# Kernel tuning notes

Hardware: AMD Instinct MI355X
Metric: run time of the kernel (lower is better)

## Reference

```python
import jax, jax.numpy as jnp
import numpy as np

N_NODES = 40000
N_EDGES = 640000
N_GRAPHS = 64
D_IN = 128
D_H = 128
N_LAYERS = 3
EPS = 1e-5


def _layer_norm(x, g, b):
    mu = jnp.mean(x, axis=-1, keepdims=True)
    var = jnp.var(x, axis=-1, keepdims=True)
    return (x - mu) * jax.lax.rsqrt(var + EPS) * g + b


def _sage_conv(x, src, dst, Wl, bl, Wr):
    # mean aggregation of neighbor messages: i <- mean_{j: (j->i)} x_j
    msg = x[src]                                              # [E, d]
    agg = jax.ops.segment_sum(msg, dst, num_segments=N_NODES)  # [N, d]
    deg = jax.ops.segment_sum(jnp.ones((src.shape[0],), x.dtype), dst,
                              num_segments=N_NODES)
    agg = agg / jnp.clip(deg, 1.0)[:, None]
    # out = lin_l(agg) + lin_r(x)
    return agg @ Wl.T + bl + x @ Wr.T


def setup_inputs() -> dict:
    key = jax.random.key(0)
    ks = jax.random.split(key, 12)
    s = 0.05
    x = jax.random.normal(ks[0], (N_NODES, D_IN), jnp.float32)
    edge_index = jax.random.randint(ks[1], (2, N_EDGES), 0, N_NODES, jnp.int64)
    batch = jnp.sort(jax.random.randint(ks[2], (N_NODES,), 0, N_GRAPHS, jnp.int64))
    fc_w = jax.random.normal(ks[3], (D_H, D_IN), jnp.float32) * s
    fc_b = jax.random.normal(ks[4], (D_H,), jnp.float32) * s
    Wl = jax.random.normal(ks[5], (N_LAYERS, D_H, D_H), jnp.float32) * s
    bl = jax.random.normal(ks[6], (N_LAYERS, D_H), jnp.float32) * s
    Wr = jax.random.normal(ks[7], (N_LAYERS, D_H, D_H), jnp.float32) * s
    ln_g = jnp.ones((N_LAYERS - 1, D_H), jnp.float32)
    ln_b = jnp.zeros((N_LAYERS - 1, D_H), jnp.float32)
    return {"x": x, "edge_index": edge_index, "batch": batch,
            "fc_w": fc_w, "fc_b": fc_b, "Wl": Wl, "bl": bl, "Wr": Wr,
            "ln_g": ln_g, "ln_b": ln_b}


def reference(x, edge_index, batch, fc_w, fc_b, Wl, bl, Wr, ln_g, ln_b):
    src, dst = edge_index[0], edge_index[1]
    # input projection + ReLU
    h = jax.nn.relu(x @ fc_w.T + fc_b)
    # GraphSAGE stack: norm + ReLU between layers, none after the last
    for i in range(N_LAYERS):
        h = _sage_conv(h, src, dst, Wl[i], bl[i], Wr[i])
        if i < N_LAYERS - 1:
            h = jax.nn.relu(_layer_norm(h, ln_g[i], ln_b[i]))
    node_embed = h                                            # [N, D_H]
    graph_embed = jax.ops.segment_sum(node_embed, batch,
                                      num_segments=N_GRAPHS)  # [G, D_H]
    return node_embed, graph_embed
```

## Files before the change

kernel.cpp:

```cpp
#include <hip/hip_runtime.h>
#include <hip/hip_bf16.h>


#define N_NODES 40000
#define N_EDGES 640000
#define N_GRAPHS 64
#define D 128
#define NODE_ELEMS 5120000
#define N_TILES 1250
#define ELL_W 64

typedef __hip_bfloat16 bf16;
typedef __attribute__((ext_vector_type(8))) short bf16x8;
typedef __attribute__((ext_vector_type(4))) float f32x4;

__device__ __forceinline__ float b2f(bf16 v) { return __bfloat162float(v); }
__device__ __forceinline__ bf16 f2b(float v) { return __float2bfloat16(v); }
__device__ __forceinline__ unsigned packbf(float a, float b) {
    union { bf16 h[2]; unsigned u; } c;
    c.h[0] = f2b(a); c.h[1] = f2b(b);
    return c.u;
}
__device__ __forceinline__ unsigned char f2e4m3(float v) {
    unsigned u = __float_as_uint(v * 0x1p-120f);
    unsigned r = (u + 0x0007ffffu + ((u >> 20) & 1u)) >> 20;
    return (unsigned char)min(r, 0x7eu);
}
__device__ __forceinline__ int is_bf16(const unsigned* lng) {
    return (lng[0] == 0x3f803f80u) ? 1 : 0;
}
__device__ __forceinline__ int edge_is_i64(const void* edge) {
    const unsigned* ew = (const unsigned*)edge;
    return (ew[1] == 0u && ew[3] == 0u && ew[5] == 0u) ? 1 : 0;
}

union U8 { uint4 u; bf16x8 s; };

template <int ISB>
__device__ __forceinline__ bf16x8 load8t(const void* base, long idx) {
    if (ISB) {
        U8 t;
        t.u = *(const uint4*)((const bf16*)base + idx);
        return t.s;
    }
    const float* f = (const float*)base + idx;
    float4 f0 = *(const float4*)f;
    float4 f1 = *(const float4*)(f + 4);
    union { bf16 h[8]; bf16x8 s; } t;
    t.h[0] = f2b(f0.x); t.h[1] = f2b(f0.y); t.h[2] = f2b(f0.z); t.h[3] = f2b(f0.w);
    t.h[4] = f2b(f1.x); t.h[5] = f2b(f1.y); t.h[6] = f2b(f1.z); t.h[7] = f2b(f1.w);
    return t.s;
}

template <int ISB>
__device__ __forceinline__ void proj_body(
    const void* __restrict__ X, const void* __restrict__ fcw,
    const void* __restrict__ fcb, bf16* __restrict__ outb,
    unsigned char* __restrict__ out8, int id, int t,
    bf16 (*sb)[128], unsigned char (*s8)[128]) {
    const int lane = t & 63;
    const int wave = t >> 6;
    const int n = lane & 15, q = lane >> 4;
    const int rowgrp = wave >> 1;
    const int cb = (wave & 1) * 64;
    const f32x4 zero = {0.f, 0.f, 0.f, 0.f};

    bf16x8 wf[4][4];
#pragma unroll
    for (int ct = 0; ct < 4; ct++)
#pragma unroll
        for (int ks = 0; ks < 4; ks++)
            wf[ct][ks] = load8t<ISB>(fcw, (long)(cb + ct * 16 + n) * 128 + ks * 32 + q * 8);
    float bz[4];
#pragma unroll
    for (int ct = 0; ct < 4; ct++)
        bz[ct] = ISB ? b2f(((const bf16*)fcb)[cb + ct * 16 + n])
                     : ((const float*)fcb)[cb + ct * 16 + n];

    for (int tile = id; tile < N_TILES; tile += 512) {
        const long rbase = (long)tile * 32 + rowgrp * 16 + n;
        f32x4 acc[4] = {zero, zero, zero, zero};
        bf16x8 af[4];
#pragma unroll
        for (int ks = 0; ks < 4; ks++)
            af[ks] = load8t<ISB>(X, rbase * 128 + ks * 32 + q * 8);
#pragma unroll
        for (int ct = 0; ct < 4; ct++)
#pragma unroll
            for (int ks = 0; ks < 4; ks++)
                acc[ct] = __builtin_amdgcn_mfma_f32_16x16x32_bf16(
                    af[ks], wf[ct][ks], acc[ct], 0, 0, 0);
#pragma unroll
        for (int ct = 0; ct < 4; ct++) {
            const int col = cb + ct * 16 + n;
#pragma unroll
            for (int r = 0; r < 4; r++) {
                const int rl = rowgrp * 16 + q * 4 + r;
                float v = fmaxf(acc[ct][r] + bz[ct], 0.f);
                sb[rl][col] = f2b(v);
                s8[rl][col] = f2e4m3(v);
            }
        }
        __syncthreads();
        {
            uint4* ob = (uint4*)((char*)outb + (size_t)tile * 8192);
            ob[t] = ((const uint4*)sb)[t];
            ob[t + 256] = ((const uint4*)sb)[t + 256];
            ((uint4*)(out8 + (size_t)tile * 4096))[t] = ((const uint4*)s8)[t];
        }
        __syncthreads();
    }
}

#define CW2_TOTAL 99200
__global__ __launch_bounds__(256, 4) void k_main(
    const void* __restrict__ X, const void* __restrict__ fcw,
    const void* __restrict__ fcb, bf16* __restrict__ outb,
    unsigned char* __restrict__ out8,
    const void* __restrict__ edge, const void* __restrict__ batch,
    const void* Wl, const void* bl, const void* Wr,
    const void* lng, const void* lnb,
    int* __restrict__ cursor, unsigned short* __restrict__ ell,
    int* __restrict__ batch32, bf16* __restrict__ cw,
    float* __restrict__ gsum) {
    __shared__ bf16 sb[32][128];
    __shared__ unsigned char s8[32][128];
    const int bid = blockIdx.x, t = threadIdx.x;
    int role, id;
    if (bid < 1000) { role = (bid & 1) ? 0 : 1; id = bid >> 1; }
    else if (bid < 1012) { role = 0; id = 500 + (bid - 1000); }
    else if (bid < 1169) { role = 2; id = bid - 1012; }
    else { role = 3; id = bid - 1169; }

    if (role == 1) {
        const int i64 = edge_is_i64(edge);
        int s[5], d[5];
#pragma unroll
        for (int i = 0; i < 5; i++) {
            int e = id * 1280 + i * 256 + t;
            if (i64) {
                s[i] = (int)((const long long*)edge)[e];
                d[i] = (int)((const long long*)edge)[N_EDGES + e];
            } else {
                s[i] = ((const int*)edge)[e];
                d[i] = ((const int*)edge)[N_EDGES + e];
            }
        }
        int p[5];
#pragma unroll
        for (int i = 0; i < 5; i++) p[i] = atomicAdd(&cursor[d[i]], 1);
#pragma unroll
        for (int i = 0; i < 5; i++)
            if (p[i] < ELL_W) ell[d[i] * ELL_W + p[i]] = (unsigned short)s[i];
        return;
    }
    if (role == 2) {
        int j = id * 256 + t;
        if (j < N_NODES)
            batch32[j] = edge_is_i64(edge) ? (int)((const long long*)batch)[j]
                                           : ((const int*)batch)[j];
        return;
    }
    if (role == 3) {
        int i = id * 256 + t;
        if (i >= CW2_TOTAL) return;
        int isb = is_bf16((const unsigned*)lng);
        const void* s; int o;
        if (i < 49152)       { s = Wl;  o = i; }
        else if (i < 49536)  { s = bl;  o = i - 49152; }
        else if (i < 98688)  { s = Wr;  o = i - 49536; }
        else if (i < 98944)  { s = lng; o = i - 98688; }
        else                 { s = lnb; o = i - 98944; }
        cw[i] = isb ? ((const bf16*)s)[o] : f2b(((const float*)s)[o]);
        return;
    }

    {
        int i = id * 256 + t;
        if (i < N_GRAPHS * D) gsum[i] = 0.f;
    }
    if (is_bf16((const unsigned*)lng))
        proj_body<1>(X, fcw, fcb, outb, out8, id, t, sb, s8);
    else
        proj_body<0>(X, fcw, fcb, outb, out8, id, t, sb, s8);
}

__global__ __launch_bounds__(256, 6) void k_agg8(
    const unsigned char* __restrict__ h8, const int* __restrict__ cursor,
    const unsigned short* __restrict__ ell, bf16* __restrict__ agg) {
    const int qw = threadIdx.x >> 4;
    const int l16 = threadIdx.x & 15;
    const int nodeA = blockIdx.x * 32 + qw * 2;
    const int nodeB = nodeA + 1;
    const int degA = min(cursor[nodeA], ELL_W);
    const int degB = min(cursor[nodeB], ELL_W);
    const int dmax = max(degA, degB);
    const uint4* rA = (const uint4*)(ell + (size_t)nodeA * ELL_W);
    const uint4* rB = (const uint4*)(ell + (size_t)nodeB * ELL_W);
    const uint2* hp = (const uint2*)h8;
    float aA[8] = {0.f, 0.f, 0.f, 0.f, 0.f, 0.f, 0.f, 0.f};
    float aB[8] = {0.f, 0.f, 0.f, 0.f, 0.f, 0.f, 0.f, 0.f};
    for (int e = 0; e < dmax; e += 8) {
        const uint4 ia = rA[e >> 3];
        const uint4 ib = rB[e >> 3];
        uint2 gA[8], gB[8];
        gA[0] = hp[(size_t)(ia.x & 0xffffu) * 16 + l16];
        gA[1] = hp[(size_t)(ia.x >> 16) * 16 + l16];
        gA[2] = hp[(size_t)(ia.y & 0xffffu) * 16 + l16];
        gA[3] = hp[(size_t)(ia.y >> 16) * 16 + l16];
        gA[4] = hp[(size_t)(ia.z & 0xffffu) * 16 + l16];
        gA[5] = hp[(size_t)(ia.z >> 16) * 16 + l16];
        gA[6] = hp[(size_t)(ia.w & 0xffffu) * 16 + l16];
        gA[7] = hp[(size_t)(ia.w >> 16) * 16 + l16];
        gB[0] = hp[(size_t)(ib.x & 0xffffu) * 16 + l16];
        gB[1] = hp[(size_t)(ib.x >> 16) * 16 + l16];
        gB[2] = hp[(size_t)(ib.y & 0xffffu) * 16 + l16];
        gB[3] = hp[(size_t)(ib.y >> 16) * 16 + l16];
        gB[4] = hp[(size_t)(ib.z & 0xffffu) * 16 + l16];
        gB[5] = hp[(size_t)(ib.z >> 16) * 16 + l16];
        gB[6] = hp[(size_t)(ib.w & 0xffffu) * 16 + l16];
        gB[7] = hp[(size_t)(ib.w >> 16) * 16 + l16];
#pragma unroll
        for (int i = 0; i < 8; i++) {
            const float mA = (e + i < degA) ? 0x1p120f : 0.f;
            aA[0] = fmaf(mA, __uint_as_float((gA[i].x << 20) & 0x07f00000u), aA[0]);
            aA[1] = fmaf(mA, __uint_as_float((gA[i].x << 12) & 0x07f00000u), aA[1]);
            aA[2] = fmaf(mA, __uint_as_float((gA[i].x << 4)  & 0x07f00000u), aA[2]);
            aA[3] = fmaf(mA, __uint_as_float((gA[i].x >> 4)  & 0x07f00000u), aA[3]);
            aA[4] = fmaf(mA, __uint_as_float((gA[i].y << 20) & 0x07f00000u), aA[4]);
            aA[5] = fmaf(mA, __uint_as_float((gA[i].y << 12) & 0x07f00000u), aA[5]);
            aA[6] = fmaf(mA, __uint_as_float((gA[i].y << 4)  & 0x07f00000u), aA[6]);
            aA[7] = fmaf(mA, __uint_as_float((gA[i].y >> 4)  & 0x07f00000u), aA[7]);
        }
#pragma unroll
        for (int i = 0; i < 8; i++) {
            const float mB = (e + i < degB) ? 0x1p120f : 0.f;
            aB[0] = fmaf(mB, __uint_as_float((gB[i].x << 20) & 0x07f00000u), aB[0]);
            aB[1] = fmaf(mB, __uint_as_float((gB[i].x << 12) & 0x07f00000u), aB[1]);
            aB[2] = fmaf(mB, __uint_as_float((gB[i].x << 4)  & 0x07f00000u), aB[2]);
            aB[3] = fmaf(mB, __uint_as_float((gB[i].x >> 4)  & 0x07f00000u), aB[3]);
            aB[4] = fmaf(mB, __uint_as_float((gB[i].y << 20) & 0x07f00000u), aB[4]);
            aB[5] = fmaf(mB, __uint_as_float((gB[i].y << 12) & 0x07f00000u), aB[5]);
            aB[6] = fmaf(mB, __uint_as_float((gB[i].y << 4)  & 0x07f00000u), aB[6]);
            aB[7] = fmaf(mB, __uint_as_float((gB[i].y >> 4)  & 0x07f00000u), aB[7]);
        }
    }
    const float invA = 1.f / (float)max(degA, 1);
    const float invB = 1.f / (float)max(degB, 1);
    uint4 oA, oB;
    oA.x = packbf(aA[0] * invA, aA[1] * invA);
    oA.y = packbf(aA[2] * invA, aA[3] * invA);
    oA.z = packbf(aA[4] * invA, aA[5] * invA);
    oA.w = packbf(aA[6] * invA, aA[7] * invA);
    oB.x = packbf(aB[0] * invB, aB[1] * invB);
    oB.y = packbf(aB[2] * invB, aB[3] * invB);
    oB.z = packbf(aB[4] * invB, aB[5] * invB);
    oB.w = packbf(aB[6] * invB, aB[7] * invB);
    ((uint4*)agg)[(size_t)nodeA * 16 + l16] = oA;
    ((uint4*)agg)[(size_t)nodeB * 16 + l16] = oB;
}

template <int MODE>
__global__ __launch_bounds__(256, 2) void k_gemm(
    const bf16* __restrict__ A, const bf16* __restrict__ W1,
    const bf16* __restrict__ B, const bf16* __restrict__ W2,
    const bf16* __restrict__ bias, bf16* __restrict__ outb,
    unsigned char* __restrict__ out8, void* __restrict__ outx,
    const bf16* __restrict__ lgam, const bf16* __restrict__ lbet,
    const unsigned* __restrict__ lngraw) {
    __shared__ float sred[2][2][16][2];
    __shared__ bf16 sb[32][128];
    __shared__ unsigned char s8[32][128];
    __shared__ float sf[32][128];
    const int tid = threadIdx.x;
    const int lane = tid & 63;
    const int wave = tid >> 6;
    const int n = lane & 15, q = lane >> 4;
    const int rowgrp = wave >> 1;
    const int cbi = wave & 1;
    const int cb = cbi * 64;
    const int isb = is_bf16(lngraw);

    bf16x8 wf[2][4][4];
#pragma unroll
    for (int p = 0; p < 2; p++) {
        const bf16* Wp = p ? W2 : W1;
#pragma unroll
        for (int ct = 0; ct < 4; ct++)
#pragma unroll
            for (int ks = 0; ks < 4; ks++) {
                U8 t;
                t.u = *(const uint4*)&Wp[(cb + ct * 16 + n) * 128 + ks * 32 + q * 8];
                wf[p][ct][ks] = t.s;
            }
    }
    float bz[4], gf[4], bf_[4];
#pragma unroll
    for (int ct = 0; ct < 4; ct++) {
        bz[ct] = b2f(bias[cb + ct * 16 + n]);
        if (MODE == 1) {
            gf[ct] = b2f(lgam[cb + ct * 16 + n]);
            bf_[ct] = b2f(lbet[cb + ct * 16 + n]);
        }
    }

    const f32x4 zero = {0.f, 0.f, 0.f, 0.f};

    for (int tile = blockIdx.x; tile < N_TILES; tile += gridDim.x) {
        const long rbase = (long)tile * 32 + rowgrp * 16 + n;
        f32x4 acc[4] = {zero, zero, zero, zero};
#pragma unroll
        for (int p = 0; p < 2; p++) {
            const bf16* Ap = p ? B : A;
            bf16x8 af[4];
#pragma unroll
            for (int ks = 0; ks < 4; ks++) {
                U8 t;
                t.u = *(const uint4*)&Ap[rbase * 128 + ks * 32 + q * 8];
                af[ks] = t.s;
            }
#pragma unroll
            for (int ct = 0; ct < 4; ct++)
#pragma unroll
                for (int ks = 0; ks < 4; ks++)
                    acc[ct] = __builtin_amdgcn_mfma_f32_16x16x32_bf16(
                        af[ks], wf[p][ct][ks], acc[ct], 0, 0, 0);
        }

        float vs[4][4];
#pragma unroll
        for (int ct = 0; ct < 4; ct++)
#pragma unroll
            for (int r = 0; r < 4; r++) vs[ct][r] = acc[ct][r] + bz[ct];

        if (MODE == 1) {
            float s[4], ss[4];
#pragma unroll
            for (int r = 0; r < 4; r++) {
                s[r] = 0.f; ss[r] = 0.f;
#pragma unroll
                for (int ct = 0; ct < 4; ct++) {
                    s[r] += vs[ct][r];
                    ss[r] += vs[ct][r] * vs[ct][r];
                }
            }
#pragma unroll
            for (int m = 1; m <= 8; m <<= 1)
#pragma unroll
                for (int r = 0; r < 4; r++) {
                    s[r] += __shfl_xor(s[r], m, 64);
                    ss[r] += __shfl_xor(ss[r], m, 64);
                }
            if (n == 0) {
#pragma unroll
                for (int r = 0; r < 4; r++) {
                    sred[rowgrp][cbi][q * 4 + r][0] = s[r];
                    sred[rowgrp][cbi][q * 4 + r][1] = ss[r];
                }
            }
            __syncthreads();
#pragma unroll
            for (int r = 0; r < 4; r++) {
                float S = s[r] + sred[rowgrp][1 - cbi][q * 4 + r][0];
                float SS = ss[r] + sred[rowgrp][1 - cbi][q * 4 + r][1];
                float mu = S * (1.f / 128.f);
                float var = SS * (1.f / 128.f) - mu * mu;
                float rstd = rsqrtf(var + 1e-5f);
#pragma unroll
                for (int ct = 0; ct < 4; ct++)
                    vs[ct][r] = fmaxf((vs[ct][r] - mu) * rstd * gf[ct] + bf_[ct], 0.f);
            }
        }

#pragma unroll
        for (int ct = 0; ct < 4; ct++) {
            const int col = cb + ct * 16 + n;
#pragma unroll
            for (int r = 0; r < 4; r++) {
                const int rl = rowgrp * 16 + q * 4 + r;
                float v = vs[ct][r];
                if (MODE == 1) {
                    sb[rl][col] = f2b(v);
                    s8[rl][col] = f2e4m3(v);
                } else {
                    if (isb) sb[rl][col] = f2b(v);
                    else sf[rl][col] = v;
                }
            }
        }
        __syncthreads();
        if (MODE == 1) {
            uint4* ob = (uint4*)((char*)outb + (size_t)tile * 8192);
            ob[tid] = ((const uint4*)sb)[tid];
            ob[tid + 256] = ((const uint4*)sb)[tid + 256];
            ((uint4*)(out8 + (size_t)tile * 4096))[tid] = ((const uint4*)s8)[tid];
        } else {
            if (isb) {
                uint4* ob = (uint4*)((char*)outx + (size_t)tile * 8192);
                ob[tid] = ((const uint4*)sb)[tid];
                ob[tid + 256] = ((const uint4*)sb)[tid + 256];
            } else {
                uint4* of = (uint4*)((char*)outx + (size_t)tile * 16384);
#pragma unroll
                for (int k = 0; k < 4; k++)
                    of[tid + 256 * k] = ((const uint4*)sf)[tid + 256 * k];
            }
        }
        __syncthreads();
    }
}

__device__ __forceinline__ int lbound(const int* a, int n, int key) {
    int lo = 0, hi = n;
    while (lo < hi) {
        int mid = (lo + hi) >> 1;
        if (a[mid] < key) lo = mid + 1; else hi = mid;
    }
    return lo;
}

__global__ void k_graph(const void* __restrict__ node, const int* __restrict__ batch,
                        float* __restrict__ gsum, const unsigned* __restrict__ lngraw) {
    const int g = blockIdx.x >> 4, part = blockIdx.x & 15;
    const int c = threadIdx.x;
    const int isb = is_bf16(lngraw);
    const int lo = lbound(batch, N_NODES, g);
    const int hi = lbound(batch, N_NODES, g + 1);
    const int len = hi - lo;
    const int b0 = lo + (len * part) / 16;
    const int b1 = lo + (len * (part + 1)) / 16;
    float s0 = 0.f, s1 = 0.f;
    int n = b0;
    if (isb) {
        const bf16* nb = (const bf16*)node;
        for (; n + 2 <= b1; n += 2) {
            s0 += b2f(nb[(size_t)(n + 0) * 128 + c]);
            s1 += b2f(nb[(size_t)(n + 1) * 128 + c]);
        }
        for (; n < b1; n++) s0 += b2f(nb[(size_t)n * 128 + c]);
    } else {
        const float* nf = (const float*)node;
        for (; n + 2 <= b1; n += 2) {
            s0 += nf[(size_t)(n + 0) * 128 + c];
            s1 += nf[(size_t)(n + 1) * 128 + c];
        }
        for (; n < b1; n++) s0 += nf[(size_t)n * 128 + c];
    }
    atomicAdd(&gsum[g * 128 + c], s0 + s1);
}

__global__ void k_gout(const float* __restrict__ gsum, void* __restrict__ out,
                       const unsigned* __restrict__ lngraw) {
    int i = blockIdx.x * 256 + threadIdx.x;
    if (i >= N_GRAPHS * D) return;
    if (is_bf16(lngraw)) ((bf16*)out)[NODE_ELEMS + i] = f2b(gsum[i]);
    else ((float*)out)[NODE_ELEMS + i] = gsum[i];
}

extern "C" void kernel_launch(void* const* d_in, const int* in_sizes, int n_in,
                              void* d_out, int out_size, void* d_ws, size_t ws_size,
                              hipStream_t stream) {
    const void* x = d_in[0];
    const void* edge = d_in[1];
    const void* batch = d_in[2];
    const void* fc_w = d_in[3];
    const void* fc_b = d_in[4];
    const void* Wl = d_in[5];
    const void* bl = d_in[6];
    const void* Wr = d_in[7];
    const void* ln_g = d_in[8];
    const void* ln_b = d_in[9];
    const unsigned* lngraw = (const unsigned*)ln_g;

    size_t off = 0;
    char* base = (char*)d_ws;
    auto carve = [&](size_t bytes) -> char* {
        char* p = base + off;
        off = (off + bytes + 255) & ~(size_t)255;
        return p;
    };
    bf16* cw = (bf16*)carve((size_t)CW2_TOTAL * 2);
    bf16* hA = (bf16*)carve((size_t)NODE_ELEMS * 2);
    bf16* hB = (bf16*)carve((size_t)NODE_ELEMS * 2);
    bf16* agg = (bf16*)carve((size_t)NODE_ELEMS * 2);
    unsigned char* h8A = (unsigned char*)carve((size_t)NODE_ELEMS);
    unsigned char* h8B = (unsigned char*)carve((size_t)NODE_ELEMS);
    int* batch32 = (int*)carve((size_t)N_NODES * 4);
    unsigned short* ell = (unsigned short*)carve((size_t)N_NODES * ELL_W * 2);
    int* cursor = (int*)carve((size_t)N_NODES * 4);
    float* gsum = (float*)carve((size_t)N_GRAPHS * D * 4);

    const bf16* cw_Wl = cw;
    const bf16* cw_bl = cw + 49152;
    const bf16* cw_Wr = cw + 49536;
    const bf16* cw_lng = cw + 98688;
    const bf16* cw_lnb = cw + 98944;

    hipMemsetAsync(cursor, 0, (size_t)N_NODES * 4, stream);
    k_main<<<1557, 256, 0, stream>>>(x, fc_w, fc_b, hA, h8A, edge, batch,
                                     Wl, bl, Wr, ln_g, ln_b,
                                     cursor, ell, batch32, cw, gsum);

    bf16* hcur = hA;
    bf16* hnext = hB;
    unsigned char* h8cur = h8A;
    unsigned char* h8next = h8B;
    for (int l = 0; l < 3; l++) {
        const bf16* W1 = cw_Wl + (size_t)l * 16384;
        const bf16* W2 = cw_Wr + (size_t)l * 16384;
        const bf16* bb = cw_bl + (size_t)l * 128;
        k_agg8<<<1250, 256, 0, stream>>>(h8cur, cursor, ell, agg);
        if (l < 2) {
            k_gemm<1><<<512, 256, 0, stream>>>(agg, W1, hcur, W2, bb, hnext,
                                               h8next, nullptr,
                                               cw_lng + (size_t)l * 128,
                                               cw_lnb + (size_t)l * 128, lngraw);
            bf16* t = hcur; hcur = hnext; hnext = t;
            unsigned char* t8 = h8cur; h8cur = h8next; h8next = t8;
        } else {
            k_gemm<2><<<512, 256, 0, stream>>>(agg, W1, hcur, W2, bb, nullptr,
                                               nullptr, d_out, nullptr, nullptr,
                                               lngraw);
        }
    }

    k_graph<<<1024, 128, 0, stream>>>(d_out, batch32, gsum, lngraw);
    k_gout<<<32, 256, 0, stream>>>(gsum, d_out, lngraw);
}
```

Measured before the change: 241.4 us.

## Store hidden states and aggregates in 8-bit float, dropping bf16 copies

Removes the bf16 copies of the node features and of the aggregated messages. Every intermediate (projection output, layer outputs, neighbor means) is now kept only in a custom 8-bit e4m3-like format and decoded to bf16 in registers before the MFMA GEMMs. This roughly halves the bytes written and read per layer in the GEMM and aggregation kernels. The cost is reduced precision for the self term and the aggregate, plus some decode ALU work in the GEMM load path.

```diff
diff --git a/kernel.cpp b/kernel.cpp
--- a/kernel.cpp
+++ b/kernel.cpp
@@ -16,11 +16,6 @@
 
 __device__ __forceinline__ float b2f(bf16 v) { return __bfloat162float(v); }
 __device__ __forceinline__ bf16 f2b(float v) { return __float2bfloat16(v); }
-__device__ __forceinline__ unsigned packbf(float a, float b) {
-    union { bf16 h[2]; unsigned u; } c;
-    c.h[0] = f2b(a); c.h[1] = f2b(b);
-    return c.u;
-}
 __device__ __forceinline__ unsigned char f2e4m3(float v) {
     unsigned u = __float_as_uint(v * 0x1p-120f);
     unsigned r = (u + 0x0007ffffu + ((u >> 20) & 1u)) >> 20;
@@ -35,6 +30,21 @@
 }
 
 union U8 { uint4 u; bf16x8 s; };
+
+__device__ __forceinline__ bf16x8 dec8(uint2 w) {
+    union { unsigned short us[8]; bf16x8 s; } o;
+#pragma unroll
+    for (int i = 0; i < 4; i++) {
+        unsigned b = (w.x >> (8 * i)) & 0xffu;
+        o.us[i] = b ? (unsigned short)((b + 960u) << 4) : (unsigned short)0;
+    }
+#pragma unroll
+    for (int i = 0; i < 4; i++) {
+        unsigned b = (w.y >> (8 * i)) & 0xffu;
+        o.us[4 + i] = b ? (unsigned short)((b + 960u) << 4) : (unsigned short)0;
+    }
+    return o.s;
+}
 
 template <int ISB>
 __device__ __forceinline__ bf16x8 load8t(const void* base, long idx) {
@@ -55,9 +65,8 @@
 template <int ISB>
 __device__ __forceinline__ void proj_body(
     const void* __restrict__ X, const void* __restrict__ fcw,
-    const void* __restrict__ fcb, bf16* __restrict__ outb,
-    unsigned char* __restrict__ out8, int id, int t,
-    bf16 (*sb)[128], unsigned char (*s8)[128]) {
+    const void* __restrict__ fcb, unsigned char* __restrict__ out8,
+    int id, int t, unsigned char (*s8)[128]) {
     const int lane = t & 63;
     const int wave = t >> 6;
     const int n = lane & 15, q = lane >> 4;
@@ -96,18 +105,11 @@
 #pragma unroll
             for (int r = 0; r < 4; r++) {
                 const int rl = rowgrp * 16 + q * 4 + r;
-                float v = fmaxf(acc[ct][r] + bz[ct], 0.f);
-                sb[rl][col] = f2b(v);
-                s8[rl][col] = f2e4m3(v);
+                s8[rl][col] = f2e4m3(fmaxf(acc[ct][r] + bz[ct], 0.f));
             }
         }
         __syncthreads();
-        {
-            uint4* ob = (uint4*)((char*)outb + (size_t)tile * 8192);
-            ob[t] = ((const uint4*)sb)[t];
-            ob[t + 256] = ((const uint4*)sb)[t + 256];
-            ((uint4*)(out8 + (size_t)tile * 4096))[t] = ((const uint4*)s8)[t];
-        }
+        ((uint4*)(out8 + (size_t)tile * 4096))[t] = ((const uint4*)s8)[t];
         __syncthreads();
     }
 }
@@ -115,15 +117,13 @@
 #define CW2_TOTAL 99200
 __global__ __launch_bounds__(256, 4) void k_main(
     const void* __restrict__ X, const void* __restrict__ fcw,
-    const void* __restrict__ fcb, bf16* __restrict__ outb,
-    unsigned char* __restrict__ out8,
+    const void* __restrict__ fcb, unsigned char* __restrict__ out8,
     const void* __restrict__ edge, const void* __restrict__ batch,
     const void* Wl, const void* bl, const void* Wr,
     const void* lng, const void* lnb,
     int* __restrict__ cursor, unsigned short* __restrict__ ell,
     int* __restrict__ batch32, bf16* __restrict__ cw,
     float* __restrict__ gsum) {
-    __shared__ bf16 sb[32][128];
     __shared__ unsigned char s8[32][128];
     const int bid = blockIdx.x, t = threadIdx.x;
     int role, id;
@@ -180,14 +180,14 @@
         if (i < N_GRAPHS * D) gsum[i] = 0.f;
     }
     if (is_bf16((const unsigned*)lng))
-        proj_body<1>(X, fcw, fcb, outb, out8, id, t, sb, s8);
+        proj_body<1>(X, fcw, fcb, out8, id, t, s8);
     else
-        proj_body<0>(X, fcw, fcb, outb, out8, id, t, sb, s8);
+        proj_body<0>(X, fcw, fcb, out8, id, t, s8);
 }
 
 __global__ __launch_bounds__(256, 6) void k_agg8(
     const unsigned char* __restrict__ h8, const int* __restrict__ cursor,
-    const unsigned short* __restrict__ ell, bf16* __restrict__ agg) {
+    const unsigned short* __restrict__ ell, unsigned char* __restrict__ agg8) {
     const int qw = threadIdx.x >> 4;
     const int l16 = threadIdx.x & 15;
     const int nodeA = blockIdx.x * 32 + qw * 2;
@@ -247,30 +247,29 @@
     }
     const float invA = 1.f / (float)max(degA, 1);
     const float invB = 1.f / (float)max(degB, 1);
-    uint4 oA, oB;
-    oA.x = packbf(aA[0] * invA, aA[1] * invA);
-    oA.y = packbf(aA[2] * invA, aA[3] * invA);
-    oA.z = packbf(aA[4] * invA, aA[5] * invA);
-    oA.w = packbf(aA[6] * invA, aA[7] * invA);
-    oB.x = packbf(aB[0] * invB, aB[1] * invB);
-    oB.y = packbf(aB[2] * invB, aB[3] * invB);
-    oB.z = packbf(aB[4] * invB, aB[5] * invB);
-    oB.w = packbf(aB[6] * invB, aB[7] * invB);
-    ((uint4*)agg)[(size_t)nodeA * 16 + l16] = oA;
-    ((uint4*)agg)[(size_t)nodeB * 16 + l16] = oB;
+    uint2 oA, oB;
+    oA.x = (unsigned)f2e4m3(aA[0] * invA) | ((unsigned)f2e4m3(aA[1] * invA) << 8) |
+           ((unsigned)f2e4m3(aA[2] * invA) << 16) | ((unsigned)f2e4m3(aA[3] * invA) << 24);
+    oA.y = (unsigned)f2e4m3(aA[4] * invA) | ((unsigned)f2e4m3(aA[5] * invA) << 8) |
+           ((unsigned)f2e4m3(aA[6] * invA) << 16) | ((unsigned)f2e4m3(aA[7] * invA) << 24);
+    oB.x = (unsigned)f2e4m3(aB[0] * invB) | ((unsigned)f2e4m3(aB[1] * invB) << 8) |
+           ((unsigned)f2e4m3(aB[2] * invB) << 16) | ((unsigned)f2e4m3(aB[3] * invB) << 24);
+    oB.y = (unsigned)f2e4m3(aB[4] * invB) | ((unsigned)f2e4m3(aB[5] * invB) << 8) |
+           ((unsigned)f2e4m3(aB[6] * invB) << 16) | ((unsigned)f2e4m3(aB[7] * invB) << 24);
+    ((uint2*)agg8)[(size_t)nodeA * 16 + l16] = oA;
+    ((uint2*)agg8)[(size_t)nodeB * 16 + l16] = oB;
 }
 
 template <int MODE>
 __global__ __launch_bounds__(256, 2) void k_gemm(
-    const bf16* __restrict__ A, const bf16* __restrict__ W1,
-    const bf16* __restrict__ B, const bf16* __restrict__ W2,
-    const bf16* __restrict__ bias, bf16* __restrict__ outb,
-    unsigned char* __restrict__ out8, void* __restrict__ outx,
-    const bf16* __restrict__ lgam, const bf16* __restrict__ lbet,
-    const unsigned* __restrict__ lngraw) {
+    const unsigned char* __restrict__ A8, const bf16* __restrict__ W1,
+    const unsigned char* __restrict__ B8, const bf16* __restrict__ W2,
+    const bf16* __restrict__ bias, unsigned char* __restrict__ out8,
+    void* __restrict__ outx, const bf16* __restrict__ lgam,
+    const bf16* __restrict__ lbet, const unsigned* __restrict__ lngraw) {
     __shared__ float sred[2][2][16][2];
+    __shared__ unsigned char s8[32][128];
     __shared__ bf16 sb[32][128];
-    __shared__ unsigned char s8[32][128];
     __shared__ float sf[32][128];
     const int tid = threadIdx.x;
     const int lane = tid & 63;
@@ -311,14 +310,11 @@
         f32x4 acc[4] = {zero, zero, zero, zero};
 #pragma unroll
         for (int p = 0; p < 2; p++) {
-            const bf16* Ap = p ? B : A;
+            const unsigned char* Ap = p ? B8 : A8;
             bf16x8 af[4];
 #pragma unroll
-            for (int ks = 0; ks < 4; ks++) {
-                U8 t;
-                t.u = *(const uint4*)&Ap[rbase * 128 + ks * 32 + q * 8];
-                af[ks] = t.s;
-            }
+            for (int ks = 0; ks < 4; ks++)
+                af[ks] = dec8(*(const uint2*)&Ap[rbase * 128 + ks * 32 + q * 8]);
 #pragma unroll
             for (int ct = 0; ct < 4; ct++)
 #pragma unroll
@@ -380,7 +376,6 @@
                 const int rl = rowgrp * 16 + q * 4 + r;
                 float v = vs[ct][r];
                 if (MODE == 1) {
-                    sb[rl][col] = f2b(v);
                     s8[rl][col] = f2e4m3(v);
                 } else {
                     if (isb) sb[rl][col] = f2b(v);
@@ -390,9 +385,6 @@
         }
         __syncthreads();
         if (MODE == 1) {
-            uint4* ob = (uint4*)((char*)outb + (size_t)tile * 8192);
-            ob[tid] = ((const uint4*)sb)[tid];
-            ob[tid + 256] = ((const uint4*)sb)[tid + 256];
             ((uint4*)(out8 + (size_t)tile * 4096))[tid] = ((const uint4*)s8)[tid];
         } else {
             if (isb) {
@@ -480,9 +472,7 @@
         return p;
     };
     bf16* cw = (bf16*)carve((size_t)CW2_TOTAL * 2);
-    bf16* hA = (bf16*)carve((size_t)NODE_ELEMS * 2);
-    bf16* hB = (bf16*)carve((size_t)NODE_ELEMS * 2);
-    bf16* agg = (bf16*)carve((size_t)NODE_ELEMS * 2);
+    unsigned char* agg8 = (unsigned char*)carve((size_t)NODE_ELEMS);
     unsigned char* h8A = (unsigned char*)carve((size_t)NODE_ELEMS);
     unsigned char* h8B = (unsigned char*)carve((size_t)NODE_ELEMS);
     int* batch32 = (int*)carve((size_t)N_NODES * 4);
@@ -497,30 +487,26 @@
     const bf16* cw_lnb = cw + 98944;
 
     hipMemsetAsync(cursor, 0, (size_t)N_NODES * 4, stream);
-    k_main<<<1557, 256, 0, stream>>>(x, fc_w, fc_b, hA, h8A, edge, batch,
+    k_main<<<1557, 256, 0, stream>>>(x, fc_w, fc_b, h8A, edge, batch,
                                      Wl, bl, Wr, ln_g, ln_b,
                                      cursor, ell, batch32, cw, gsum);
 
-    bf16* hcur = hA;
-    bf16* hnext = hB;
     unsigned char* h8cur = h8A;
     unsigned char* h8next = h8B;
     for (int l = 0; l < 3; l++) {
         const bf16* W1 = cw_Wl + (size_t)l * 16384;
         const bf16* W2 = cw_Wr + (size_t)l * 16384;
         const bf16* bb = cw_bl + (size_t)l * 128;
-        k_agg8<<<1250, 256, 0, stream>>>(h8cur, cursor, ell, agg);
+        k_agg8<<<1250, 256, 0, stream>>>(h8cur, cursor, ell, agg8);
         if (l < 2) {
-            k_gemm<1><<<512, 256, 0, stream>>>(agg, W1, hcur, W2, bb, hnext,
-                                               h8next, nullptr,
+            k_gemm<1><<<512, 256, 0, stream>>>(agg8, W1, h8cur, W2, bb, h8next,
+                                               nullptr,
                                                cw_lng + (size_t)l * 128,
                                                cw_lnb + (size_t)l * 128, lngraw);
-            bf16* t = hcur; hcur = hnext; hnext = t;
             unsigned char* t8 = h8cur; h8cur = h8next; h8next = t8;
         } else {
-            k_gemm<2><<<512, 256, 0, stream>>>(agg, W1, hcur, W2, bb, nullptr,
-                                               nullptr, d_out, nullptr, nullptr,
-                                               lngraw);
+            k_gemm<2><<<512, 256, 0, stream>>>(agg8, W1, h8cur, W2, bb, nullptr,
+                                               d_out, nullptr, nullptr, lngraw);
         }
     }
 
```

Measured after the change: 242.7 us. No clear change (+0.6%).
